# Kernel optimization log

Measured on AMD Instinct MI355X. Metric: run time of the kernel, lower is better.

## Reference

```python
import jax, jax.numpy as jnp
import numpy as np

# Fixed reactor dimensions and grey-box constants (from hyb_greybox_pars / xuyscales)
NX, NU, NY, NP = 3, 1, 2, 4
NZ = NP * (NY + NU)          # 12
F, V, DELTA = 0.1, 1.0, 1.0
CAMEAN, CBMEAN = 1.0, 0.5    # yscale mean
CASTD, CBSTD = 0.5, 0.3      # yscale std
CAFMEAN, CAFSTD = 2.0, 0.5   # uscale


def _fnn(x, layers):
    """Feed-forward NN: tanh hidden layers, linear output layer."""
    for W, b in layers[:-1]:
        x = jnp.tanh(x @ W + b)
    W, b = layers[-1]
    return x @ W + b


def setup_inputs() -> dict:
    key = jax.random.key(0)
    ks = jax.random.split(key, 16)
    B, T = 2048, 1024
    d = {
        "useq": jax.random.normal(ks[0], (B, T, NU), jnp.float32),
        "x0": 0.1 * jax.random.normal(ks[1], (B, NX + NZ), jnp.float32),
    }
    s1 = 1.0 / np.sqrt(1.0)
    s16 = 1.0 / np.sqrt(16.0)
    s12 = 1.0 / np.sqrt(12.0)
    s32 = 1.0 / np.sqrt(32.0)
    for i, name in enumerate(["r1", "r2", "r3"]):
        d[name + "_W0"] = s1 * jax.random.normal(ks[2 + 2 * i], (1, 16), jnp.float32)
        d[name + "_b0"] = jnp.zeros((16,), jnp.float32)
        d[name + "_W1"] = s16 * jax.random.normal(ks[3 + 2 * i], (16, 1), jnp.float32)
        d[name + "_b1"] = jnp.zeros((1,), jnp.float32)
    d["estC_W0"] = s12 * jax.random.normal(ks[10], (12, 32), jnp.float32)
    d["estC_b0"] = jnp.zeros((32,), jnp.float32)
    d["estC_W1"] = s32 * jax.random.normal(ks[11], (32, 1), jnp.float32)
    d["estC_b1"] = jnp.zeros((1,), jnp.float32)
    return d


def reference(useq, x0,
              r1_W0, r1_b0, r1_W1, r1_b1,
              r2_W0, r2_b0, r2_W1, r2_b1,
              r3_W0, r3_b0, r3_W1, r3_b1,
              estC_W0, estC_b0, estC_W1, estC_b1):
    r1L = [(r1_W0, r1_b0), (r1_W1, r1_b1)]
    r2L = [(r2_W0, r2_b0), (r2_W1, r2_b1)]
    r3L = [(r3_W0, r3_b0), (r3_W1, r3_b1)]
    estCL = [(estC_W0, estC_b0), (estC_W1, estC_b1)]

    def fxu(x, u):
        Ca, Cb, Cc = x[:, 0:1], x[:, 1:2], x[:, 2:3]
        Caf = u[:, 0:1]
        r1 = _fnn(Ca, r1L) * CASTD
        r2 = _fnn(Cb, r2L) * CBSTD
        r3 = _fnn(Cc, r3L) * CBSTD
        Ca = Ca * CASTD + CAMEAN
        Cb = Cb * CBSTD + CBMEAN
        Cc = Cc * CBSTD + CBMEAN
        Caf = Caf * CAFSTD + CAFMEAN
        dCa = F * (Caf - Ca) / V - r1
        dCb = -F * Cb / V + r1 - 3.0 * r2 + r3
        dCc = -F * Cc / V + r2 - r3
        return jnp.concatenate([dCa / CASTD, dCb / CBSTD, dCc / CBSTD], axis=-1)

    def step(xz, u):
        x, z = xz[:, :NX], xz[:, NX:]
        ypseq, upseq = z[:, :NP * NY], z[:, NP * NY:]
        k1 = fxu(x, u)
        k2 = fxu(x + DELTA * (k1 / 2.0), u)
        k3 = fxu(x + DELTA * (k2 / 2.0), u)
        k4 = fxu(x + DELTA * k3, u)
        xplus = x + (DELTA / 6.0) * (k1 + 2.0 * k2 + 2.0 * k3 + k4)
        zplus = jnp.concatenate([ypseq[:, NY:], x[:, :NY], upseq[:, NU:], u], axis=-1)
        CcNN = _fnn(z, estCL)
        y = jnp.concatenate([x, CcNN], axis=-1)   # [B, Ny + 2*numUnmeasGb] = [B, 4]
        return jnp.concatenate([xplus, zplus], axis=-1), y

    u_t = jnp.swapaxes(useq, 0, 1)                # [T, B, Nu]
    _, ys = jax.lax.scan(step, x0, u_t)           # ys: [T, B, 4]
    return jnp.swapaxes(ys, 0, 1)                 # [B, T, 4]
```

## Files before the change

### kernel.cpp

```cpp
#include <hip/hip_runtime.h>

#define TT 1024
#define BB 2048
#define L2E2 2.8853900817779268f

typedef float v2f __attribute__((ext_vector_type(2)));

template <int CTRL>
__device__ __forceinline__ float dpp_add(float x) {
  int y = __builtin_amdgcn_update_dpp(0, __float_as_int(x), CTRL, 0xF, 0xF, true);
  return x + __int_as_float(y);
}
template <int CTRL>
__device__ __forceinline__ float dpp_mov(float x) {
  int y = __builtin_amdgcn_update_dpp(0, __float_as_int(x), CTRL, 0xF, 0xF, true);
  return __int_as_float(y);
}
__device__ __forceinline__ float sum8(float x) {
  x = dpp_add<0xB1>(x);
  x = dpp_add<0x4E>(x);
  x = dpp_add<0x141>(x);
  return x;
}
__device__ __forceinline__ float rdlane(float x, int l) {
  return __int_as_float(__builtin_amdgcn_readlane(__float_as_int(x), l));
}
__device__ __forceinline__ v2f pkfma(float s, v2f w, v2f a) {
  return __builtin_elementwise_fma((v2f){s, s}, w, a);
}

__global__ __launch_bounds__(256) void phase1_kernel(
    const float* __restrict__ useq, const float* __restrict__ x0,
    const float* __restrict__ r1W0, const float* __restrict__ r1b0,
    const float* __restrict__ r1W1, const float* __restrict__ r1b1,
    const float* __restrict__ r2W0, const float* __restrict__ r2b0,
    const float* __restrict__ r2W1, const float* __restrict__ r2b1,
    const float* __restrict__ r3W0, const float* __restrict__ r3b0,
    const float* __restrict__ r3W1, const float* __restrict__ r3b1,
    float* __restrict__ out) {
  const int lane = threadIdx.x & 63;
  const int eh = lane >> 5;
  const int g = (lane >> 3) & 3;
  const int i = lane & 7;
  const int e0 = __builtin_amdgcn_readfirstlane(
      (blockIdx.x * 4 + (threadIdx.x >> 6)) * 2);
  const int e = e0 + eh;

  const float* W0p = (g == 1) ? r1W0 : (g == 0) ? r2W0 : r3W0;
  const float* b0p = (g == 1) ? r1b0 : (g == 0) ? r2b0 : r3b0;
  const float* W1p = (g == 1) ? r1W1 : (g == 0) ? r2W1 : r3W1;

  const v2f w0s = {W0p[i] * L2E2, W0p[i + 8] * L2E2};
  const v2f b0s = {b0p[i] * L2E2, b0p[i + 8] * L2E2};
  const v2f iwn = {1.0f / (-2.0f * W1p[i]),
                   1.0f / (-2.0f * W1p[i + 8])};

  float C1 = r1b1[0], C2 = r2b1[0], C3 = r3b1[0];
  for (int q = 0; q < 16; ++q) {
    C1 += r1W1[q];
    C2 += r2W1[q];
    C3 += r3W1[q];
  }
  const float caC = 0.2f - C1;
  const float cbC = -1.0f / 6.0f + (5.0f / 3.0f) * C1 - 3.0f * C2 + C3;
  const float ccC = -1.0f / 6.0f + C2 - C3;

  const int srow = (g == 1) ? 0 : (g == 0) ? 1 : 2;
  const float cstBase = (g == 1) ? caC : (g == 0) ? cbC : ccC;
  const float uco = (g == 1) ? 0.1f : 0.0f;
  const float c0 = (g == 0) ? -3.0f : -1.0f;
  const float c1 = (g == 0) ? (5.0f / 3.0f) : 0.0f;
  const float cR3a = (g == 0 && eh == 0) ? 1.0f : 0.0f;
  const float cR3b = (g == 0 && eh == 1) ? 1.0f : 0.0f;
  const float cR2a = (g >= 2 && eh == 0) ? 1.0f : 0.0f;
  const float cR2b = (g >= 2 && eh == 1) ? 1.0f : 0.0f;

  float S = x0[e * 15 + srow];

  const float* up0 = useq + e0 * TT;
  const float* up1 = useq + (e0 + 1) * TT;
  float* op = out + (size_t)e * TT * 4 + srow;
  const bool sflag = (i == 0 && g < 3);

#define STAGE(SS, KK)                                                     \
  {                                                                       \
    v2f h = __builtin_elementwise_fma(w0s, (v2f){(SS), (SS)}, b0s);       \
    h.x = __builtin_amdgcn_exp2f(h.x);                                    \
    h.y = __builtin_amdgcn_exp2f(h.y);                                    \
    h = __builtin_elementwise_fma(h, iwn, iwn);                           \
    float rv = __builtin_amdgcn_rcpf(h.x) + __builtin_amdgcn_rcpf(h.y);   \
    float q = sum8(rv);                                                   \
    float sP2a = rdlane(q, 0);                                            \
    float sP3a = rdlane(q, 16);                                           \
    float sP2b = rdlane(q, 32);                                           \
    float sP3b = rdlane(q, 48);                                           \
    float t_ = fmaf(-0.1f, (SS), cstS);                                   \
    t_ = fmaf(c0, q, t_);                                                 \
    t_ = fmaf(c1, dpp_mov<0x128>(q), t_);                                 \
    t_ = fmaf(cR3a, sP3a, t_);                                            \
    t_ = fmaf(cR3b, sP3b, t_);                                            \
    t_ = fmaf(cR2a, sP2a, t_);                                            \
    t_ = fmaf(cR2b, sP2b, t_);                                            \
    KK = t_;                                                              \
  }

#define STEP(UA, UB, SC_)                                                 \
  {                                                                       \
    const float usel = eh ? (UB) : (UA);                                  \
    const float cstS = fmaf(uco, usel, cstBase);                          \
    SC_ = S;                                                              \
    float k1, k2, k3, k4;                                                 \
    STAGE(S, k1)                                                          \
    float s2 = fmaf(0.5f, k1, S);                                         \
    STAGE(s2, k2)                                                         \
    float s3 = fmaf(0.5f, k2, S);                                         \
    STAGE(s3, k3)                                                         \
    float s4 = S + k3;                                                    \
    STAGE(s4, k4)                                                         \
    S = fmaf(1.0f / 6.0f, fmaf(2.0f, k2 + k3, k1) + k4, S);               \
  }

  float4 cura = *(const float4*)(up0);
  float4 curb = *(const float4*)(up1);

  for (int t0 = 0; t0 < TT; t0 += 4) {
    const int tn = (t0 + 4 <= TT - 4) ? (t0 + 4) : (TT - 4);
    const float4 naa = *(const float4*)(up0 + tn);
    const float4 nab = *(const float4*)(up1 + tn);

    float sc0, sc1, sc2, sc3;
    STEP(cura.x, curb.x, sc0)
    STEP(cura.y, curb.y, sc1)
    STEP(cura.z, curb.z, sc2)
    STEP(cura.w, curb.w, sc3)

    if (sflag) {
      float* p = op + t0 * 4;
      p[0] = sc0;  p[4] = sc1;  p[8] = sc2;  p[12] = sc3;
    }

    cura = naa;
    curb = nab;
  }
#undef STEP
#undef STAGE
}

__global__ __launch_bounds__(256) void phase2_kernel(
    const float* __restrict__ useq, const float* __restrict__ x0,
    const float* __restrict__ W0, const float* __restrict__ b0,
    const float* __restrict__ W1, const float* __restrict__ b1p,
    float* __restrict__ out) {
  __shared__ float4 wq[16][8];
  if (threadIdx.x < 128) {
    const int p = threadIdx.x >> 3, q = threadIdx.x & 7;
    float4 v = {0.0f, 0.0f, 0.0f, 0.0f};
    if (q < 6) {
      v.x = W0[(2 * q) * 32 + 2 * p] * L2E2;
      v.y = W0[(2 * q) * 32 + 2 * p + 1] * L2E2;
      v.z = W0[(2 * q + 1) * 32 + 2 * p] * L2E2;
      v.w = W0[(2 * q + 1) * 32 + 2 * p + 1] * L2E2;
    } else if (q == 6) {
      v.x = b0[2 * p] * L2E2;
      v.y = b0[2 * p + 1] * L2E2;
      v.z = -2.0f * W1[2 * p];
      v.w = -2.0f * W1[2 * p + 1];
    }
    wq[p][q] = v;
  }
  __syncthreads();

  float base = b1p[0];
#pragma unroll
  for (int h = 0; h < 32; ++h) base += W1[h];

  const int b = blockIdx.x * 2 + (threadIdx.x >> 7);
  const int tid = threadIdx.x & 127;
  const int t0 = tid * 8;
  const float* xrow = x0 + b * 15;

  v2f hy[11];
  float hu[11];
  if (tid != 0) {
    const float* py = out + ((size_t)(b << 10) + t0 - 4) * 4;
#pragma unroll
    for (int i = 0; i < 11; ++i) hy[i] = *(const v2f*)(py + i * 4);
    const float* pu = useq + (b << 10) + t0 - 4;
    const float4 ua = *(const float4*)(pu);
    const float4 ub = *(const float4*)(pu + 4);
    const float4 uc = *(const float4*)(pu + 8);
    hu[0] = ua.x; hu[1] = ua.y; hu[2] = ua.z; hu[3] = ua.w;
    hu[4] = ub.x; hu[5] = ub.y; hu[6] = ub.z; hu[7] = ub.w;
    hu[8] = uc.x; hu[9] = uc.y; hu[10] = uc.z;
  } else {
#pragma unroll
    for (int i = 0; i < 4; ++i) {
      hy[i] = (v2f){xrow[3 + 2 * i], xrow[4 + 2 * i]};
      hu[i] = xrow[11 + i];
    }
    const float* py = out + ((size_t)(b << 10)) * 4;
    const float* pu = useq + (b << 10);
#pragma unroll
    for (int i = 4; i < 11; ++i) {
      hy[i] = *(const v2f*)(py + (i - 4) * 4);
      hu[i] = pu[i - 4];
    }
  }

  float ov[8];
#pragma unroll
  for (int k = 0; k < 8; ++k) ov[k] = base;

#pragma unroll
  for (int p = 0; p < 16; ++p) {
    const float4 w01 = wq[p][0];
    const float4 w23 = wq[p][1];
    const float4 w45 = wq[p][2];
    const float4 w67 = wq[p][3];
    const float4 wu01 = wq[p][4];
    const float4 wu23 = wq[p][5];
    const float4 wb = wq[p][6];
#define ACC2(OV, ZY, ZU)                                                  \
  {                                                                       \
    v2f a = (v2f){wb.x, wb.y};                                            \
    a = pkfma((ZY)[0].x, (v2f){w01.x, w01.y}, a);                         \
    a = pkfma((ZY)[0].y, (v2f){w01.z, w01.w}, a);                         \
    a = pkfma((ZY)[1].x, (v2f){w23.x, w23.y}, a);                         \
    a = pkfma((ZY)[1].y, (v2f){w23.z, w23.w}, a);                         \
    a = pkfma((ZY)[2].x, (v2f){w45.x, w45.y}, a);                         \
    a = pkfma((ZY)[2].y, (v2f){w45.z, w45.w}, a);                         \
    a = pkfma((ZY)[3].x, (v2f){w67.x, w67.y}, a);                         \
    a = pkfma((ZY)[3].y, (v2f){w67.z, w67.w}, a);                         \
    a = pkfma((ZU)[0], (v2f){wu01.x, wu01.y}, a);                         \
    a = pkfma((ZU)[1], (v2f){wu01.z, wu01.w}, a);                         \
    a = pkfma((ZU)[2], (v2f){wu23.x, wu23.y}, a);                         \
    a = pkfma((ZU)[3], (v2f){wu23.z, wu23.w}, a);                         \
    const float sx =                                                      \
        __builtin_amdgcn_rcpf(__builtin_amdgcn_exp2f(a.x) + 1.0f);        \
    const float sy =                                                      \
        __builtin_amdgcn_rcpf(__builtin_amdgcn_exp2f(a.y) + 1.0f);        \
    OV = fmaf(wb.z, sx, OV);                                              \
    OV = fmaf(wb.w, sy, OV);                                              \
  }
#pragma unroll
    for (int k = 0; k < 8; ++k) ACC2(ov[k], (&hy[k]), (&hu[k]))
#undef ACC2
  }

  float* po = out + ((size_t)(b << 10) + t0) * 4 + 3;
#pragma unroll
  for (int k = 0; k < 8; ++k) po[4 * k] = ov[k];
}

extern "C" void kernel_launch(void* const* d_in, const int* in_sizes, int n_in,
                              void* d_out, int out_size, void* d_ws,
                              size_t ws_size, hipStream_t stream) {
  const float* useq = (const float*)d_in[0];
  const float* x0 = (const float*)d_in[1];
  float* out = (float*)d_out;

  phase1_kernel<<<BB / 8, 256, 0, stream>>>(
      useq, x0,
      (const float*)d_in[2], (const float*)d_in[3], (const float*)d_in[4],
      (const float*)d_in[5], (const float*)d_in[6], (const float*)d_in[7],
      (const float*)d_in[8], (const float*)d_in[9], (const float*)d_in[10],
      (const float*)d_in[11], (const float*)d_in[12], (const float*)d_in[13],
      out);

  phase2_kernel<<<BB / 2, 256, 0, stream>>>(
      useq, x0, (const float*)d_in[14], (const float*)d_in[15],
      (const float*)d_in[16], (const float*)d_in[17], out);
}
```

Baseline: 428.9 us.

## Fuse estimator MLP into the sequential RK4 kernel and drop phase2 launch

Removes the separate phase2 kernel that re-read the stored trajectory to evaluate the 12->32->1 estimator network. Instead, each lane of the RK4 recurrence kernel evaluates one hidden unit per step from a register-resident shift window of past outputs and inputs, reduces across 32 lanes with DPP, and writes the fourth output column directly. This avoids the extra launch and the global re-read of outputs. In exchange, the latency-bound serial step loop gains an FMA chain, an exp/rcp and a longer cross-lane reduction per step.

```diff
diff --git a/kernel.cpp b/kernel.cpp
--- a/kernel.cpp
+++ b/kernel.cpp
@@ -24,9 +24,6 @@
 }
 __device__ __forceinline__ float rdlane(float x, int l) {
   return __int_as_float(__builtin_amdgcn_readlane(__float_as_int(x), l));
-}
-__device__ __forceinline__ v2f pkfma(float s, v2f w, v2f a) {
-  return __builtin_elementwise_fma((v2f){s, s}, w, a);
 }
 
 __global__ __launch_bounds__(256) void phase1_kernel(
@@ -37,6 +34,8 @@
     const float* __restrict__ r2W1, const float* __restrict__ r2b1,
     const float* __restrict__ r3W0, const float* __restrict__ r3b0,
     const float* __restrict__ r3W1, const float* __restrict__ r3b1,
+    const float* __restrict__ eW0, const float* __restrict__ eb0p,
+    const float* __restrict__ eW1, const float* __restrict__ eb1p,
     float* __restrict__ out) {
   const int lane = threadIdx.x & 63;
   const int eh = lane >> 5;
@@ -65,7 +64,7 @@
   const float cbC = -1.0f / 6.0f + (5.0f / 3.0f) * C1 - 3.0f * C2 + C3;
   const float ccC = -1.0f / 6.0f + C2 - C3;
 
-  const int srow = (g == 1) ? 0 : (g == 0) ? 1 : 2;
+  const int strow = (g == 1) ? 0 : (g == 0) ? 1 : 2;
   const float cstBase = (g == 1) ? caC : (g == 0) ? cbC : ccC;
   const float uco = (g == 1) ? 0.1f : 0.0f;
   const float c0 = (g == 0) ? -3.0f : -1.0f;
@@ -75,12 +74,38 @@
   const float cR2a = (g >= 2 && eh == 0) ? 1.0f : 0.0f;
   const float cR2b = (g >= 2 && eh == 1) ? 1.0f : 0.0f;
 
-  float S = x0[e * 15 + srow];
+  float S = x0[e * 15 + strow];
+
+  const int n = lane & 31;
+  const float eb0v = eb0p[n] * L2E2;
+  const float ew0 = eW0[0 * 32 + n] * L2E2;
+  const float ew1 = eW0[1 * 32 + n] * L2E2;
+  const float ew2 = eW0[2 * 32 + n] * L2E2;
+  const float ew3 = eW0[3 * 32 + n] * L2E2;
+  const float ew4 = eW0[4 * 32 + n] * L2E2;
+  const float ew5 = eW0[5 * 32 + n] * L2E2;
+  const float ew6 = eW0[6 * 32 + n] * L2E2;
+  const float ew7 = eW0[7 * 32 + n] * L2E2;
+  const float ew8 = eW0[8 * 32 + n] * L2E2;
+  const float ew9 = eW0[9 * 32 + n] * L2E2;
+  const float ew10 = eW0[10 * 32 + n] * L2E2;
+  const float ew11 = eW0[11 * 32 + n] * L2E2;
+  const float ew1n = -2.0f * eW1[n];
+  float ebs = eb1p[0];
+  for (int q = 0; q < 32; ++q) ebs += eW1[q];
+  const float eb32 = ebs * 0.03125f;
+
+  const float* zp = x0 + e * 15 + 3;
+  float hA0 = zp[0], hB0 = zp[1], hA1 = zp[2], hB1 = zp[3];
+  float hA2 = zp[4], hB2 = zp[5], hA3 = zp[6], hB3 = zp[7];
+  float hU0 = zp[8], hU1 = zp[9], hU2 = zp[10], hU3 = zp[11];
 
   const float* up0 = useq + e0 * TT;
   const float* up1 = useq + (e0 + 1) * TT;
-  float* op = out + (size_t)e * TT * 4 + srow;
-  const bool sflag = (i == 0 && g < 3);
+  const int soff = (g == 1) ? 0 : (g == 0) ? 1 : (g == 2) ? 2 : 3;
+  float* op = out + (size_t)e * TT * 4 + soff;
+  const bool sflag = (i == 0);
+  const bool isg3 = (g == 3);
 
 #define STAGE(SS, KK)                                                     \
   {                                                                       \
@@ -104,11 +129,38 @@
     KK = t_;                                                              \
   }
 
-#define STEP(UA, UB, SC_)                                                 \
+#define STEP(UA, UB, SC_, hA0_, hB0_, hA1_, hB1_, hA2_, hB2_, hA3_, hB3_, \
+             hU0_, hU1_, hU2_, hU3_, NA_, NB_, NU_)                       \
   {                                                                       \
-    const float usel = eh ? (UB) : (UA);                                  \
-    const float cstS = fmaf(uco, usel, cstBase);                          \
-    SC_ = S;                                                              \
+    float a_ = fmaf((hA0_), ew0, eb0v);                                   \
+    a_ = fmaf((hB0_), ew1, a_);                                           \
+    a_ = fmaf((hA1_), ew2, a_);                                           \
+    a_ = fmaf((hB1_), ew3, a_);                                           \
+    a_ = fmaf((hA2_), ew4, a_);                                           \
+    a_ = fmaf((hB2_), ew5, a_);                                           \
+    a_ = fmaf((hA3_), ew6, a_);                                           \
+    a_ = fmaf((hB3_), ew7, a_);                                           \
+    a_ = fmaf((hU0_), ew8, a_);                                           \
+    a_ = fmaf((hU1_), ew9, a_);                                           \
+    a_ = fmaf((hU2_), ew10, a_);                                          \
+    a_ = fmaf((hU3_), ew11, a_);                                          \
+    float er_ = __builtin_amdgcn_rcpf(__builtin_amdgcn_exp2f(a_) + 1.0f); \
+    float ps_ = fmaf(ew1n, er_, eb32);                                    \
+    ps_ = dpp_add<0xB1>(ps_);                                             \
+    ps_ = dpp_add<0x4E>(ps_);                                             \
+    ps_ = dpp_add<0x141>(ps_);                                            \
+    ps_ = dpp_add<0x140>(ps_);                       \
+    ps_ = dpp_add<0x142>(ps_);         \
+    const float sBa_ = rdlane(S, 0);                                      \
+    const float sAa_ = rdlane(S, 8);                                      \
+    const float sBb_ = rdlane(S, 32);                                     \
+    const float sAb_ = rdlane(S, 40);                                     \
+    NA_ = eh ? sAb_ : sAa_;                                               \
+    NB_ = eh ? sBb_ : sBa_;                                               \
+    const float usel_ = eh ? (UB) : (UA);                                 \
+    NU_ = usel_;                                                          \
+    const float cstS = fmaf(uco, usel_, cstBase);                         \
+    SC_ = isg3 ? ps_ : S;                                                 \
     float k1, k2, k3, k4;                                                 \
     STAGE(S, k1)                                                          \
     float s2 = fmaf(0.5f, k1, S);                                         \
@@ -129,127 +181,30 @@
     const float4 nab = *(const float4*)(up1 + tn);
 
     float sc0, sc1, sc2, sc3;
-    STEP(cura.x, curb.x, sc0)
-    STEP(cura.y, curb.y, sc1)
-    STEP(cura.z, curb.z, sc2)
-    STEP(cura.w, curb.w, sc3)
+    float A4, B4, U4, A5, B5, U5, A6, B6, U6, A7, B7, U7;
+    STEP(cura.x, curb.x, sc0, hA0, hB0, hA1, hB1, hA2, hB2, hA3, hB3,
+         hU0, hU1, hU2, hU3, A4, B4, U4)
+    STEP(cura.y, curb.y, sc1, hA1, hB1, hA2, hB2, hA3, hB3, A4, B4,
+         hU1, hU2, hU3, U4, A5, B5, U5)
+    STEP(cura.z, curb.z, sc2, hA2, hB2, hA3, hB3, A4, B4, A5, B5,
+         hU2, hU3, U4, U5, A6, B6, U6)
+    STEP(cura.w, curb.w, sc3, hA3, hB3, A4, B4, A5, B5, A6, B6,
+         hU3, U4, U5, U6, A7, B7, U7)
 
     if (sflag) {
       float* p = op + t0 * 4;
       p[0] = sc0;  p[4] = sc1;  p[8] = sc2;  p[12] = sc3;
     }
 
+    hA0 = A4; hB0 = B4; hA1 = A5; hB1 = B5;
+    hA2 = A6; hB2 = B6; hA3 = A7; hB3 = B7;
+    hU0 = U4; hU1 = U5; hU2 = U6; hU3 = U7;
+
     cura = naa;
     curb = nab;
   }
 #undef STEP
 #undef STAGE
-}
-
-__global__ __launch_bounds__(256) void phase2_kernel(
-    const float* __restrict__ useq, const float* __restrict__ x0,
-    const float* __restrict__ W0, const float* __restrict__ b0,
-    const float* __restrict__ W1, const float* __restrict__ b1p,
-    float* __restrict__ out) {
-  __shared__ float4 wq[16][8];
-  if (threadIdx.x < 128) {
-    const int p = threadIdx.x >> 3, q = threadIdx.x & 7;
-    float4 v = {0.0f, 0.0f, 0.0f, 0.0f};
-    if (q < 6) {
-      v.x = W0[(2 * q) * 32 + 2 * p] * L2E2;
-      v.y = W0[(2 * q) * 32 + 2 * p + 1] * L2E2;
-      v.z = W0[(2 * q + 1) * 32 + 2 * p] * L2E2;
-      v.w = W0[(2 * q + 1) * 32 + 2 * p + 1] * L2E2;
-    } else if (q == 6) {
-      v.x = b0[2 * p] * L2E2;
-      v.y = b0[2 * p + 1] * L2E2;
-      v.z = -2.0f * W1[2 * p];
-      v.w = -2.0f * W1[2 * p + 1];
-    }
-    wq[p][q] = v;
-  }
-  __syncthreads();
-
-  float base = b1p[0];
-#pragma unroll
-  for (int h = 0; h < 32; ++h) base += W1[h];
-
-  const int b = blockIdx.x * 2 + (threadIdx.x >> 7);
-  const int tid = threadIdx.x & 127;
-  const int t0 = tid * 8;
-  const float* xrow = x0 + b * 15;
-
-  v2f hy[11];
-  float hu[11];
-  if (tid != 0) {
-    const float* py = out + ((size_t)(b << 10) + t0 - 4) * 4;
-#pragma unroll
-    for (int i = 0; i < 11; ++i) hy[i] = *(const v2f*)(py + i * 4);
-    const float* pu = useq + (b << 10) + t0 - 4;
-    const float4 ua = *(const float4*)(pu);
-    const float4 ub = *(const float4*)(pu + 4);
-    const float4 uc = *(const float4*)(pu + 8);
-    hu[0] = ua.x; hu[1] = ua.y; hu[2] = ua.z; hu[3] = ua.w;
-    hu[4] = ub.x; hu[5] = ub.y; hu[6] = ub.z; hu[7] = ub.w;
-    hu[8] = uc.x; hu[9] = uc.y; hu[10] = uc.z;
-  } else {
-#pragma unroll
-    for (int i = 0; i < 4; ++i) {
-      hy[i] = (v2f){xrow[3 + 2 * i], xrow[4 + 2 * i]};
-      hu[i] = xrow[11 + i];
-    }
-    const float* py = out + ((size_t)(b << 10)) * 4;
-    const float* pu = useq + (b << 10);
-#pragma unroll
-    for (int i = 4; i < 11; ++i) {
-      hy[i] = *(const v2f*)(py + (i - 4) * 4);
-      hu[i] = pu[i - 4];
-    }
-  }
-
-  float ov[8];
-#pragma unroll
-  for (int k = 0; k < 8; ++k) ov[k] = base;
-
-#pragma unroll
-  for (int p = 0; p < 16; ++p) {
-    const float4 w01 = wq[p][0];
-    const float4 w23 = wq[p][1];
-    const float4 w45 = wq[p][2];
-    const float4 w67 = wq[p][3];
-    const float4 wu01 = wq[p][4];
-    const float4 wu23 = wq[p][5];
-    const float4 wb = wq[p][6];
-#define ACC2(OV, ZY, ZU)                                                  \
-  {                                                                       \
-    v2f a = (v2f){wb.x, wb.y};                                            \
-    a = pkfma((ZY)[0].x, (v2f){w01.x, w01.y}, a);                         \
-    a = pkfma((ZY)[0].y, (v2f){w01.z, w01.w}, a);                         \
-    a = pkfma((ZY)[1].x, (v2f){w23.x, w23.y}, a);                         \
-    a = pkfma((ZY)[1].y, (v2f){w23.z, w23.w}, a);                         \
-    a = pkfma((ZY)[2].x, (v2f){w45.x, w45.y}, a);                         \
-    a = pkfma((ZY)[2].y, (v2f){w45.z, w45.w}, a);                         \
-    a = pkfma((ZY)[3].x, (v2f){w67.x, w67.y}, a);                         \
-    a = pkfma((ZY)[3].y, (v2f){w67.z, w67.w}, a);                         \
-    a = pkfma((ZU)[0], (v2f){wu01.x, wu01.y}, a);                         \
-    a = pkfma((ZU)[1], (v2f){wu01.z, wu01.w}, a);                         \
-    a = pkfma((ZU)[2], (v2f){wu23.x, wu23.y}, a);                         \
-    a = pkfma((ZU)[3], (v2f){wu23.z, wu23.w}, a);                         \
-    const float sx =                                                      \
-        __builtin_amdgcn_rcpf(__builtin_amdgcn_exp2f(a.x) + 1.0f);        \
-    const float sy =                                                      \
-        __builtin_amdgcn_rcpf(__builtin_amdgcn_exp2f(a.y) + 1.0f);        \
-    OV = fmaf(wb.z, sx, OV);                                              \
-    OV = fmaf(wb.w, sy, OV);                                              \
-  }
-#pragma unroll
-    for (int k = 0; k < 8; ++k) ACC2(ov[k], (&hy[k]), (&hu[k]))
-#undef ACC2
-  }
-
-  float* po = out + ((size_t)(b << 10) + t0) * 4 + 3;
-#pragma unroll
-  for (int k = 0; k < 8; ++k) po[4 * k] = ov[k];
 }
 
 extern "C" void kernel_launch(void* const* d_in, const int* in_sizes, int n_in,
@@ -265,9 +220,6 @@
       (const float*)d_in[5], (const float*)d_in[6], (const float*)d_in[7],
       (const float*)d_in[8], (const float*)d_in[9], (const float*)d_in[10],
       (const float*)d_in[11], (const float*)d_in[12], (const float*)d_in[13],
-      out);
-
-  phase2_kernel<<<BB / 2, 256, 0, stream>>>(
-      useq, x0, (const float*)d_in[14], (const float*)d_in[15],
-      (const float*)d_in[16], (const float*)d_in[17], out);
-}
+      (const float*)d_in[14], (const float*)d_in[15], (const float*)d_in[16],
+      (const float*)d_in[17], out);
+}
```

Result: no change. 426.9 us (-0.5%).
